# Performance work log

Measured on AMD Instinct MI355X. Metric: run time of the kernel, lower is better.

The kernel has to match this reference:

```python
import jax, jax.numpy as jnp
import numpy as np
from jax import lax

WS = 8        # window size
NH = 4        # num heads
HD = 32       # head dim
DIM = NH * HD # 128
SCALE = HD ** -0.5


def _rel_index(ws):
    coords = np.stack(np.meshgrid(np.arange(ws), np.arange(ws), indexing='ij'))  # (2,ws,ws)
    cf = coords.reshape(2, -1)                      # (2, N)
    rel = cf[:, :, None] - cf[:, None, :]           # (2, N, N)
    rel = rel.transpose(1, 2, 0).astype(np.int64)   # (N, N, 2)
    rel[..., 0] += ws - 1
    rel[..., 1] += ws - 1
    rel[..., 0] *= 2 * ws - 1
    return jnp.asarray(rel.sum(-1))                 # (N, N)


def setup_inputs() -> dict:
    key = jax.random.key(0)
    ks = jax.random.split(key, 8)
    B, H, W = 8, 128, 128
    return {
        'x': jax.random.normal(ks[0], (B, DIM, H, W), jnp.float32),
        'qkv_w': jax.random.normal(ks[1], (DIM, 3 * DIM), jnp.float32) * 0.02,
        'qkv_b': jnp.zeros((3 * DIM,), jnp.float32),
        'proj_w': jax.random.normal(ks[2], (DIM, DIM), jnp.float32) * 0.02,
        'proj_b': jnp.zeros((DIM,), jnp.float32),
        'rpb_table': jax.random.normal(ks[3], ((2 * WS - 1) * (2 * WS - 1), NH), jnp.float32) * 0.02,
        'fc_w': jax.random.normal(ks[4], (9, 3 * NH), jnp.float32) * 0.1,   # 1x1 conv: (out=9, in=3*NH)
        'fc_b': jnp.zeros((9,), jnp.float32),
        'dep_w': jax.random.normal(ks[5], (DIM, 9, 3, 3), jnp.float32) * 0.1,  # grouped conv OIHW, groups=HD
        'dep_b': jnp.zeros((DIM,), jnp.float32),
        'rate1': jnp.array(0.5, jnp.float32),
        'rate2': jnp.array(0.5, jnp.float32),
    }


def reference(x, qkv_w, qkv_b, proj_w, proj_b, rpb_table, fc_w, fc_b, dep_w, dep_b, rate1, rate2):
    B, C, H, W = x.shape
    N = WS * WS
    xh = jnp.transpose(x, (0, 2, 3, 1))                 # (B,H,W,C)
    qkv = xh @ qkv_w + qkv_b                            # (B,H,W,3C)

    # ----- conv branch -----
    f_all = qkv.reshape(B, H * W, 3 * NH, HD).transpose(0, 2, 1, 3)       # (B,3NH,HW,HD)
    f_c = jnp.einsum('oc,bcnd->bond', fc_w, f_all) + fc_b[None, :, None, None]  # (B,9,HW,HD)
    f_conv = jnp.transpose(f_c, (0, 3, 1, 2)).reshape(B, HD * 9, H, W)    # (B,9*HD,H,W)
    out_conv = lax.conv_general_dilated(
        f_conv, dep_w, window_strides=(1, 1), padding=((1, 1), (1, 1)),
        dimension_numbers=('NCHW', 'OIHW', 'NCHW'), feature_group_count=HD)
    out_conv = jnp.transpose(out_conv + dep_b[None, :, None, None], (0, 2, 3, 1))  # (B,H,W,C)

    # ----- windowed attention branch -----
    nWh, nWw = H // WS, W // WS
    w = qkv.reshape(B, nWh, WS, nWw, WS, 3 * C).transpose(0, 1, 3, 2, 4, 5)
    w = w.reshape(B * nWh * nWw, N, 3, NH, HD).transpose(2, 0, 3, 1, 4)   # (3,Bw,NH,N,HD)
    q, k, v = w[0] * SCALE, w[1], w[2]
    attn = jnp.einsum('bhnd,bhmd->bhnm', q, k)                            # (Bw,NH,N,N)
    bias = rpb_table[_rel_index(WS)]                                      # (N,N,NH)
    attn = attn + jnp.transpose(bias, (2, 0, 1))[None]
    attn = jax.nn.softmax(attn, axis=-1)
    xa = jnp.einsum('bhnm,bhmd->bnhd', attn, v).reshape(-1, N, C)         # (Bw,N,C)
    xa = xa @ proj_w + proj_b
    xa = xa.reshape(B, nWh, nWw, WS, WS, C).transpose(0, 1, 3, 2, 4, 5).reshape(B, H, W, C)

    out = rate1 * xa + rate2 * out_conv
    return jnp.transpose(out, (0, 3, 1, 2))
```

## Files before the change

kernel.cpp:

```cpp
#include <hip/hip_runtime.h>

typedef unsigned short ushort_t;
typedef unsigned int uint_t;
typedef __attribute__((ext_vector_type(8))) short short8;
typedef __attribute__((ext_vector_type(4))) float f32x4;

#define SCALE 0.17677669529663687f

__device__ __forceinline__ float blo(uint_t u) { return __uint_as_float(u << 16); }
__device__ __forceinline__ float bhi(uint_t u) { return __uint_as_float(u & 0xffff0000u); }
__device__ __forceinline__ float u2f(ushort_t u) { return __uint_as_float(((uint_t)u) << 16); }
__device__ __forceinline__ ushort_t f2u(float f) {
    const uint_t x = __float_as_uint(f);
    return (ushort_t)((x + 0x7fffu + ((x >> 16) & 1u)) >> 16);
}
__device__ __forceinline__ uint_t pack2(float a, float b) {
    return (uint_t)f2u(a) | ((uint_t)f2u(b) << 16);
}

__device__ __forceinline__ float dot8(const float* qa, uint4 u) {
    return qa[0] * blo(u.x) + qa[1] * bhi(u.x) + qa[2] * blo(u.y) + qa[3] * bhi(u.y)
         + qa[4] * blo(u.z) + qa[5] * bhi(u.z) + qa[6] * blo(u.w) + qa[7] * bhi(u.w);
}
__device__ __forceinline__ void pv8(float* a, float e, uint4 u) {
    a[0] += e * blo(u.x); a[1] += e * bhi(u.x); a[2] += e * blo(u.y); a[3] += e * bhi(u.y);
    a[4] += e * blo(u.z); a[5] += e * bhi(u.z); a[6] += e * blo(u.w); a[7] += e * bhi(u.w);
}


__global__ __launch_bounds__(256) void k_qqkv(
    const float* __restrict__ x, const float* __restrict__ w,
    const float* __restrict__ wb, ushort_t* __restrict__ qkv)
{
    __shared__ ushort_t XT[128 * 128];
    __shared__ ushort_t WT[128 * 128];
    const int t = threadIdx.x;
    const int p0 = blockIdx.x * 128;
    const int b = p0 >> 14;
    const int rem = p0 & 16383;
    const float* xb = x + ((size_t)b << 21) + rem;

#pragma unroll
    for (int it = 0; it < 8; ++it) {
        const int slot = it * 256 + t;
        const int p = slot & 127, cb = slot >> 7;
        uint4 u;
        {
            const float a0 = xb[(size_t)(cb * 8 + 0) * 16384 + p];
            const float a1 = xb[(size_t)(cb * 8 + 1) * 16384 + p];
            const float a2 = xb[(size_t)(cb * 8 + 2) * 16384 + p];
            const float a3 = xb[(size_t)(cb * 8 + 3) * 16384 + p];
            const float a4 = xb[(size_t)(cb * 8 + 4) * 16384 + p];
            const float a5 = xb[(size_t)(cb * 8 + 5) * 16384 + p];
            const float a6 = xb[(size_t)(cb * 8 + 6) * 16384 + p];
            const float a7 = xb[(size_t)(cb * 8 + 7) * 16384 + p];
            u.x = pack2(a0, a1); u.y = pack2(a2, a3);
            u.z = pack2(a4, a5); u.w = pack2(a6, a7);
        }
        *(uint4*)&XT[p * 128 + ((cb ^ (p & 7)) << 3)] = u;
    }

    const int l = t & 63, wv = t >> 6;
    const int wj = (wv >> 1) * 64, wp = (wv & 1) * 64;
    const int lr = l & 15, lg = l >> 4;

    for (int jt = 0; jt < 3; ++jt) {
        const int j0 = jt * 128;
        __syncthreads();

#pragma unroll
        for (int it = 0; it < 8; ++it) {
            const int slot = it * 256 + t;
            const int j = slot & 127, cb = slot >> 7;
            uint4 u;
            {
                const float a0 = w[(size_t)(cb * 8 + 0) * 384 + j0 + j];
                const float a1 = w[(size_t)(cb * 8 + 1) * 384 + j0 + j];
                const float a2 = w[(size_t)(cb * 8 + 2) * 384 + j0 + j];
                const float a3 = w[(size_t)(cb * 8 + 3) * 384 + j0 + j];
                const float a4 = w[(size_t)(cb * 8 + 4) * 384 + j0 + j];
                const float a5 = w[(size_t)(cb * 8 + 5) * 384 + j0 + j];
                const float a6 = w[(size_t)(cb * 8 + 6) * 384 + j0 + j];
                const float a7 = w[(size_t)(cb * 8 + 7) * 384 + j0 + j];
                u.x = pack2(a0, a1); u.y = pack2(a2, a3);
                u.z = pack2(a4, a5); u.w = pack2(a6, a7);
            }
            *(uint4*)&WT[j * 128 + ((cb ^ (j & 7)) << 3)] = u;
        }
        __syncthreads();

        f32x4 acc[4][4];
#pragma unroll
        for (int i = 0; i < 4; ++i)
#pragma unroll
            for (int j = 0; j < 4; ++j) acc[i][j] = (f32x4){0.f, 0.f, 0.f, 0.f};

#pragma unroll
        for (int ks = 0; ks < 4; ++ks) {
            const int kb = ks * 4 + lg;
            short8 af[4], bf[4];
#pragma unroll
            for (int i = 0; i < 4; ++i) {
                const int jr = wj + i * 16 + lr;
                af[i] = *(const short8*)&WT[jr * 128 + ((kb ^ (jr & 7)) << 3)];
                const int pr = wp + i * 16 + lr;
                bf[i] = *(const short8*)&XT[pr * 128 + ((kb ^ (pr & 7)) << 3)];
            }
#pragma unroll
            for (int ji = 0; ji < 4; ++ji)
#pragma unroll
                for (int pi = 0; pi < 4; ++pi)
                    acc[ji][pi] = __builtin_amdgcn_mfma_f32_16x16x32_bf16(
                        af[ji], bf[pi], acc[ji][pi], 0, 0, 0);
        }
        __syncthreads();

#pragma unroll
        for (int ji = 0; ji < 4; ++ji) {
            const int jq = wj + ji * 16 + 4 * lg;
            const float4 bias = *(const float4*)&wb[j0 + jq];
#pragma unroll
            for (int pi = 0; pi < 4; ++pi) {
                const int p = wp + pi * 16 + lr;
                uint2 o;
                o.x = pack2(acc[ji][pi][0] + bias.x, acc[ji][pi][1] + bias.y);
                o.y = pack2(acc[ji][pi][2] + bias.z, acc[ji][pi][3] + bias.w);
                *(uint2*)&WT[p * 128 + (((jq >> 3) ^ (p & 7)) << 3) + (jq & 7)] = o;
            }
        }
        __syncthreads();

#pragma unroll
        for (int it = 0; it < 8; ++it) {
            const int slot = it * 256 + t;
            const int seg = slot & 15, p = slot >> 4;
            const uint4 v = *(const uint4*)&WT[p * 128 + ((seg ^ (p & 7)) << 3)];
            *(uint4*)&qkv[(size_t)(p0 + p) * 384 + j0 + seg * 8] = v;
        }
    }
}

__global__ __launch_bounds__(256, 4) void k_attn3(
    const ushort_t* __restrict__ qkv, const float* __restrict__ rpb,
    float* __restrict__ out)
{
    __shared__ float arena[9604];
    uint_t* kv32 = (uint_t*)arena;
    float* rpbl = arena + 8704;
    const int t = threadIdx.x;
    const int b = blockIdx.x >> 8, wy = (blockIdx.x >> 4) & 15, wx = blockIdx.x & 15;
    const int prow0 = (b << 14) + (wy * 8) * 128 + wx * 8;
    const uint_t* qkvu = (const uint_t*)qkv;

    for (int i = t; i < 4096; i += 256) {
        const int m = i >> 6, u = i & 63;
        const size_t pr = (size_t)(prow0 + (m >> 3) * 128 + (m & 7)) * 192;
        kv32[m * 68 + u]        = qkvu[pr + 64 + u];
        kv32[4352 + m * 68 + u] = qkvu[pr + 128 + u];
    }
    for (int i = t; i < 900; i += 256) rpbl[i] = rpb[i];

    const int h = t >> 6, n = t & 63;
    const size_t pq = (size_t)(prow0 + (n >> 3) * 128 + (n & 7)) * 192;
    float qa[32];
    const uint_t* qrow = qkvu + pq + h * 16;
#pragma unroll
    for (int j = 0; j < 16; ++j) {
        const uint_t u = qrow[j];
        qa[2 * j]     = blo(u) * SCALE;
        qa[2 * j + 1] = bhi(u) * SCALE;
    }
    __syncthreads();

    const int ry = n >> 3, rx = n & 7;
    const float* rpbl_t = rpbl + h;
    const int rbase = (ry + 7) * 15 + (rx + 7);

    const uint_t* kbase = kv32 + h * 16;
    const uint_t* vbase = kv32 + 4352 + h * 16;

    float mx = -1e30f, l = 0.f;
    float acc[32];
#pragma unroll
    for (int cc = 0; cc < 32; ++cc) acc[cc] = 0.f;

#pragma unroll 4
    for (int m = 0; m < 64; ++m) {
        const uint4* kr = (const uint4*)(kbase + m * 68);
        const uint4 k0 = kr[0], k1 = kr[1], k2 = kr[2], k3 = kr[3];
        float s = (dot8(qa, k0) + dot8(qa + 8, k1))
                + (dot8(qa + 16, k2) + dot8(qa + 24, k3));
        s += rpbl_t[4 * (rbase - (m >> 3) * 15 - (m & 7))];
        if (s > mx) {
            const float sc = __expf(mx - s);
            mx = s;
            l *= sc;
#pragma unroll
            for (int cc = 0; cc < 32; ++cc) acc[cc] *= sc;
        }
        const float e = __expf(s - mx);
        l += e;
        const uint4* vr = (const uint4*)(vbase + m * 68);
        const uint4 v0 = vr[0], v1 = vr[1], v2 = vr[2], v3 = vr[3];
        pv8(acc, e, v0); pv8(acc + 8, e, v1);
        pv8(acc + 16, e, v2); pv8(acc + 24, e, v3);
    }
    const float inv = 1.f / l;

    const int oy = wy * 8 + ry, ox = wx * 8 + rx;
    float* ob = out + ((size_t)b << 21) + (size_t)(oy * 128 + ox);
#pragma unroll
    for (int cc = 0; cc < 32; ++cc)
        ob[(size_t)(h * 32 + cc) << 14] = acc[cc] * inv;
}

__global__ __launch_bounds__(256) void k_proj(
    const float* __restrict__ pw, const float* __restrict__ pb,
    const float* __restrict__ r1, float* __restrict__ out)
{
    __shared__ ushort_t XT[128 * 128];
    __shared__ ushort_t WT[128 * 128];
    const int t = threadIdx.x;
    const int p0 = blockIdx.x * 128;
    const int b = p0 >> 14;
    const int rem = p0 & 16383;
    const float* xb = out + ((size_t)b << 21) + rem;

#pragma unroll
    for (int it = 0; it < 8; ++it) {
        const int slot = it * 256 + t;
        const int p = slot & 127, cb = slot >> 7;
        uint4 u;
        {
            const float a0 = xb[(size_t)(cb * 8 + 0) * 16384 + p];
            const float a1 = xb[(size_t)(cb * 8 + 1) * 16384 + p];
            const float a2 = xb[(size_t)(cb * 8 + 2) * 16384 + p];
            const float a3 = xb[(size_t)(cb * 8 + 3) * 16384 + p];
            const float a4 = xb[(size_t)(cb * 8 + 4) * 16384 + p];
            const float a5 = xb[(size_t)(cb * 8 + 5) * 16384 + p];
            const float a6 = xb[(size_t)(cb * 8 + 6) * 16384 + p];
            const float a7 = xb[(size_t)(cb * 8 + 7) * 16384 + p];
            u.x = pack2(a0, a1); u.y = pack2(a2, a3);
            u.z = pack2(a4, a5); u.w = pack2(a6, a7);
        }
        *(uint4*)&XT[p * 128 + ((cb ^ (p & 7)) << 3)] = u;
    }
#pragma unroll
    for (int it = 0; it < 8; ++it) {
        const int slot = it * 256 + t;
        const int j = slot & 127, cb = slot >> 7;
        uint4 u;
        {
            const float a0 = pw[(size_t)(cb * 8 + 0) * 128 + j];
            const float a1 = pw[(size_t)(cb * 8 + 1) * 128 + j];
            const float a2 = pw[(size_t)(cb * 8 + 2) * 128 + j];
            const float a3 = pw[(size_t)(cb * 8 + 3) * 128 + j];
            const float a4 = pw[(size_t)(cb * 8 + 4) * 128 + j];
            const float a5 = pw[(size_t)(cb * 8 + 5) * 128 + j];
            const float a6 = pw[(size_t)(cb * 8 + 6) * 128 + j];
            const float a7 = pw[(size_t)(cb * 8 + 7) * 128 + j];
            u.x = pack2(a0, a1); u.y = pack2(a2, a3);
            u.z = pack2(a4, a5); u.w = pack2(a6, a7);
        }
        *(uint4*)&WT[j * 128 + ((cb ^ (j & 7)) << 3)] = u;
    }
    __syncthreads();

    const int l = t & 63, wv = t >> 6;
    const int wj = (wv >> 1) * 64, wp = (wv & 1) * 64;
    const int lr = l & 15, lg = l >> 4;

    f32x4 acc[4][4];
#pragma unroll
    for (int i = 0; i < 4; ++i)
#pragma unroll
        for (int j = 0; j < 4; ++j) acc[i][j] = (f32x4){0.f, 0.f, 0.f, 0.f};

#pragma unroll
    for (int ks = 0; ks < 4; ++ks) {
        const int kb = ks * 4 + lg;
        short8 af[4], bf[4];
#pragma unroll
        for (int i = 0; i < 4; ++i) {
            const int jr = wj + i * 16 + lr;
            af[i] = *(const short8*)&WT[jr * 128 + ((kb ^ (jr & 7)) << 3)];
            const int pr = wp + i * 16 + lr;
            bf[i] = *(const short8*)&XT[pr * 128 + ((kb ^ (pr & 7)) << 3)];
        }
#pragma unroll
        for (int ji = 0; ji < 4; ++ji)
#pragma unroll
            for (int pi = 0; pi < 4; ++pi)
                acc[ji][pi] = __builtin_amdgcn_mfma_f32_16x16x32_bf16(
                    af[ji], bf[pi], acc[ji][pi], 0, 0, 0);
    }

    const float rate1 = r1[0];
    float* obase = out + ((size_t)b << 21) + rem;
#pragma unroll
    for (int ji = 0; ji < 4; ++ji) {
        const int jq = wj + ji * 16 + 4 * lg;
        const float4 bias = *(const float4*)&pb[jq];
#pragma unroll
        for (int pi = 0; pi < 4; ++pi) {
            const int p = wp + pi * 16 + lr;
            float* op = obase + (size_t)jq * 16384 + p;
            op[0]     = rate1 * (acc[ji][pi][0] + bias.x);
            op[16384] = rate1 * (acc[ji][pi][1] + bias.y);
            op[32768] = rate1 * (acc[ji][pi][2] + bias.z);
            op[49152] = rate1 * (acc[ji][pi][3] + bias.w);
        }
    }
}

__global__ __launch_bounds__(256) void k_conv2(
    const ushort_t* __restrict__ qkv, const float* __restrict__ fcw,
    const float* __restrict__ fcb, const float* __restrict__ depw,
    const float* __restrict__ depb, const float* __restrict__ r2,
    float* __restrict__ out)
{
    __shared__ float fcl[11664];
    __shared__ __align__(16) float dwl[1296];
    __shared__ float fcwl[108];
    __shared__ float fcbl[9];

    const int t = threadIdx.x;
    const int b = blockIdx.x >> 6, tile = blockIdx.x & 63;
    const int ty0 = (tile >> 3) << 4, tx0 = (tile & 7) << 4;
    if (t < 108) fcwl[t] = fcw[t];
    if (t < 9)   fcbl[t] = fcb[t];
    const float rate2 = r2[0];
    const int py = t >> 4, px = t & 15;
    float* ob = out + ((size_t)b << 21) + (size_t)((ty0 + py) * 128 + (tx0 + px));

    const int row0 = t / 18, col0 = t - row0 * 18;
    const int hy0 = ty0 + row0 - 1, hx0 = tx0 + col0 - 1;
    const int g0 = ((unsigned)hy0 < 128u && (unsigned)hx0 < 128u)
                       ? ((b << 14) + hy0 * 128 + hx0) : -1;
    const int t1 = t + 256, row1 = t1 / 18, col1 = t1 - row1 * 18;
    const int hy1 = ty0 + row1 - 1, hx1 = tx0 + col1 - 1;
    const int g1 = (t < 68 && (unsigned)hy1 < 128u && (unsigned)hx1 < 128u)
                       ? ((b << 14) + hy1 * 128 + hx1) : -1;

    for (int chunk = 0; chunk < 8; ++chunk) {
        __syncthreads();
        for (int i = t; i < 1296; i += 256)
            dwl[i] = depw[(chunk * 16 + (i & 15)) * 81 + (i >> 4)];

#pragma unroll
        for (int half = 0; half < 2; ++half) {
            const int g = half ? g1 : g0;
            const int pix = half ? (256 + t) : t;
            if (half && t >= 68) break;
            float fo[9][4];
#pragma unroll
            for (int ii = 0; ii < 9; ++ii) {
                const float bv = (g >= 0) ? fcbl[ii] : 0.f;
                fo[ii][0] = bv; fo[ii][1] = bv; fo[ii][2] = bv; fo[ii][3] = bv;
            }
            if (g >= 0) {
                const uint2* qp = (const uint2*)(qkv + (size_t)g * 384 + chunk * 4);
#pragma unroll
                for (int e = 0; e < 12; ++e) {
                    const uint2 q = qp[e * 8];
                    const float f0 = blo(q.x), f1 = bhi(q.x);
                    const float f2 = blo(q.y), f3 = bhi(q.y);
#pragma unroll
                    for (int ii = 0; ii < 9; ++ii) {
                        const float wv = fcwl[ii * 12 + e];
                        fo[ii][0] += wv * f0; fo[ii][1] += wv * f1;
                        fo[ii][2] += wv * f2; fo[ii][3] += wv * f3;
                    }
                }
            }
#pragma unroll
            for (int ii = 0; ii < 9; ++ii)
#pragma unroll
                for (int dd = 0; dd < 4; ++dd)
                    fcl[(ii * 4 + dd) * 324 + pix] = fo[ii][dd];
        }
        __syncthreads();

        float4 accv[4];
#pragma unroll
        for (int dd = 0; dd < 4; ++dd) accv[dd] = make_float4(0.f, 0.f, 0.f, 0.f);
#pragma unroll
        for (int ii = 0; ii < 9; ++ii) {
#pragma unroll
            for (int kk = 0; kk < 9; ++kk) {
                const int ky = kk / 3, kx = kk - (kk / 3) * 3;
                const int hpix = (py + ky) * 18 + px + kx;
                const float4* dwp = (const float4*)&dwl[(ii * 9 + kk) * 16];
#pragma unroll
                for (int dd = 0; dd < 4; ++dd) {
                    const float f = fcl[(ii * 4 + dd) * 324 + hpix];
                    const float4 d4 = dwp[dd];
                    accv[dd].x += f * d4.x; accv[dd].y += f * d4.y;
                    accv[dd].z += f * d4.z; accv[dd].w += f * d4.w;
                }
            }
        }
#pragma unroll
        for (int dd = 0; dd < 4; ++dd) {
            const float av[4] = {accv[dd].x, accv[dd].y, accv[dd].z, accv[dd].w};
#pragma unroll
            for (int j = 0; j < 4; ++j) {
                const int oc = chunk * 16 + dd * 4 + j;
                ob[(size_t)oc << 14] += rate2 * (av[j] + depb[oc]);
            }
        }
    }
}

#define WS_W2  0
#define WS_B2  36864
#define WS_TOT 37152

__global__ __launch_bounds__(256) void k_prep_f(
    const float* __restrict__ qkv_w, const float* __restrict__ qkv_b,
    const float* __restrict__ fcw, const float* __restrict__ fcb,
    float* __restrict__ ws)
{
    const int idx = blockIdx.x * 256 + threadIdx.x;
    if (idx < WS_B2) {
        const int c = idx / 288, r = idx - c * 288, i = r >> 5, d = r & 31;
        float s = 0.f;
#pragma unroll
        for (int e = 0; e < 12; ++e)
            s += fcw[i * 12 + e] * qkv_w[c * 384 + e * 32 + d];
        ws[idx] = s;
    } else if (idx < WS_TOT) {
        const int r = idx - WS_B2, i = r >> 5, d = r & 31;
        float s = fcb[i];
#pragma unroll
        for (int e = 0; e < 12; ++e)
            s += fcw[i * 12 + e] * qkv_b[e * 32 + d];
        ws[idx] = s;
    }
}

__global__ __launch_bounds__(256) void k_attn_f(
    const float* __restrict__ x, const float* __restrict__ qw,
    const float* __restrict__ qb, const float* __restrict__ pw,
    const float* __restrict__ pb, const float* __restrict__ rpb,
    const float* __restrict__ r1, float* __restrict__ out)
{
    __shared__ ushort_t xw[8192];
    __shared__ float arena[8450];
    ushort_t* kvb = (ushort_t*)arena;
    const int t = threadIdx.x;
    const int b = blockIdx.x >> 8, wy = (blockIdx.x >> 4) & 15, wx = blockIdx.x & 15;
    const size_t xbase = ((size_t)b << 21) + (size_t)((wy * 8) * 128 + wx * 8);
    for (int i = t; i < 8192; i += 256) {
        const int c = i >> 6, p = i & 63;
        xw[i] = f2u(x[xbase + (size_t)c * 16384 + (p >> 3) * 128 + (p & 7)]);
    }
    __syncthreads();
    const int h = t >> 6, n = t & 63;
    float qa[32], ka[32], va[32];
#pragma unroll
    for (int cc = 0; cc < 32; ++cc) {
        qa[cc] = qb[h * 32 + cc];
        ka[cc] = qb[128 + h * 32 + cc];
        va[cc] = qb[256 + h * 32 + cc];
    }
    const float* wbase = qw + h * 32;
    for (int c = 0; c < 128; ++c) {
        const float xv = u2f(xw[c * 64 + n]);
        const float* wr = wbase + c * 384;
#pragma unroll
        for (int j = 0; j < 8; ++j) {
            const float4 aq = ((const float4*)wr)[j];
            const float4 ak = ((const float4*)(wr + 128))[j];
            const float4 av = ((const float4*)(wr + 256))[j];
            qa[4 * j + 0] += xv * aq.x; qa[4 * j + 1] += xv * aq.y;
            qa[4 * j + 2] += xv * aq.z; qa[4 * j + 3] += xv * aq.w;
            ka[4 * j + 0] += xv * ak.x; ka[4 * j + 1] += xv * ak.y;
            ka[4 * j + 2] += xv * ak.z; ka[4 * j + 3] += xv * ak.w;
            va[4 * j + 0] += xv * av.x; va[4 * j + 1] += xv * av.y;
            va[4 * j + 2] += xv * av.z; va[4 * j + 3] += xv * av.w;
        }
    }
#pragma unroll
    for (int cc = 0; cc < 32; ++cc) qa[cc] *= SCALE;
    uint_t* kv32 = (uint_t*)kvb;
#pragma unroll
    for (int j = 0; j < 16; ++j) {
        kv32[n * 66 + h * 16 + j] = pack2(ka[2 * j], ka[2 * j + 1]);
        kv32[4224 + n * 66 + h * 16 + j] = pack2(va[2 * j], va[2 * j + 1]);
    }
    __syncthreads();
    const int ry = n >> 3, rx = n & 7;
    float sar[64];
    float mx = -1e30f;
#pragma unroll
    for (int m = 0; m < 64; ++m) {
        const uint2* kr = (const uint2*)(kvb + m * 132 + h * 32);
        float s = 0.f;
#pragma unroll
        for (int j = 0; j < 8; ++j) {
            const uint2 u = kr[j];
            s += qa[4 * j + 0] * blo(u.x) + qa[4 * j + 1] * bhi(u.x)
               + qa[4 * j + 2] * blo(u.y) + qa[4 * j + 3] * bhi(u.y);
        }
        s += rpb[((ry - (m >> 3) + 7) * 15 + (rx - (m & 7) + 7)) * 4 + h];
        sar[m] = s;
        mx = fmaxf(mx, s);
    }
    float l = 0.f;
#pragma unroll
    for (int m = 0; m < 64; ++m) { const float e = __expf(sar[m] - mx); sar[m] = e; l += e; }
    const float inv = 1.f / l;
    float acc[32];
#pragma unroll
    for (int cc = 0; cc < 32; ++cc) acc[cc] = 0.f;
#pragma unroll
    for (int m = 0; m < 64; ++m) {
        const float pm = sar[m];
        const uint2* vr = (const uint2*)(kvb + 8448 + m * 132 + h * 32);
#pragma unroll
        for (int j = 0; j < 8; ++j) {
            const uint2 u = vr[j];
            acc[4 * j + 0] += pm * blo(u.x); acc[4 * j + 1] += pm * bhi(u.x);
            acc[4 * j + 2] += pm * blo(u.y); acc[4 * j + 3] += pm * bhi(u.y);
        }
    }
    __syncthreads();
#pragma unroll
    for (int cc = 0; cc < 32; ++cc) arena[n * 130 + h * 32 + cc] = acc[cc] * inv;
    __syncthreads();
    const int p = t & 63, jb = t >> 6;
    float aj[32];
#pragma unroll
    for (int jj = 0; jj < 32; ++jj) aj[jj] = pb[jb * 32 + jj];
    const float* xr = arena + p * 130;
    const float* pwb = pw + jb * 32;
    for (int c = 0; c < 128; ++c) {
        const float xv = xr[c];
        const float4* pr = (const float4*)(pwb + c * 128);
#pragma unroll
        for (int j = 0; j < 8; ++j) {
            const float4 w4 = pr[j];
            aj[4 * j + 0] += xv * w4.x; aj[4 * j + 1] += xv * w4.y;
            aj[4 * j + 2] += xv * w4.z; aj[4 * j + 3] += xv * w4.w;
        }
    }
    const float rate1 = r1[0];
    const int oy = wy * 8 + (p >> 3), ox = wx * 8 + (p & 7);
    float* ob = out + ((size_t)b << 21) + (size_t)(oy * 128 + ox);
#pragma unroll
    for (int jj = 0; jj < 32; ++jj)
        ob[(size_t)(jb * 32 + jj) << 14] = rate1 * aj[jj];
}

__global__ __launch_bounds__(256) void k_conv_f(
    const float* __restrict__ x, const float* __restrict__ ws,
    const float* __restrict__ depw, const float* __restrict__ depb,
    const float* __restrict__ r2, float* __restrict__ out)
{
    __shared__ float arena[12960];
    __shared__ float b2s[36];
    float* w2l = arena;
    ushort_t* xl = (ushort_t*)(arena + 4608);
    float* fcl = arena;
    float* dwl = arena + 11664;
    const int t = threadIdx.x;
    const int b = blockIdx.x >> 6, tile = blockIdx.x & 63;
    const int ty0 = (tile >> 3) << 4, tx0 = (tile & 7) << 4;
    const size_t xbase = ((size_t)b << 21);
    const float rate2 = r2[0];
    const int py = t >> 4, px = t & 15;
    float* ob = out + ((size_t)b << 21) + (size_t)((ty0 + py) * 128 + (tx0 + px));
    const int r0 = t / 18, c0 = t - r0 * 18;
    const bool ok0 = ((unsigned)(ty0 + r0 - 1) < 128u) && ((unsigned)(tx0 + c0 - 1) < 128u);
    const int t1 = 256 + t, r1i = t1 / 18, c1 = t1 - r1i * 18;
    const bool ok1 = (t < 68) && ((unsigned)(ty0 + r1i - 1) < 128u) && ((unsigned)(tx0 + c1 - 1) < 128u);
    for (int chunk = 0; chunk < 8; ++chunk) {
        __syncthreads();
        for (int i = t; i < 4608; i += 256) {
            const int c = i / 36, r = i - c * 36;
            w2l[i] = ws[WS_W2 + c * 288 + (r >> 2) * 32 + chunk * 4 + (r & 3)];
        }
        if (t < 36) b2s[t] = ws[WS_B2 + (t >> 2) * 32 + chunk * 4 + (t & 3)];
        __syncthreads();
        float fca[2][36];
#pragma unroll
        for (int r = 0; r < 36; ++r) { fca[0][r] = b2s[r]; fca[1][r] = b2s[r]; }
        for (int cs = 0; cs < 8; ++cs) {
            if (cs) __syncthreads();
            for (int i = t; i < 5184; i += 256) {
                const int cc = i / 324, pp = i - cc * 324;
                const int row = pp / 18, col = pp - row * 18;
                const int hy = ty0 + row - 1, hx = tx0 + col - 1;
                ushort_t v = 0;
                if ((unsigned)hy < 128u && (unsigned)hx < 128u)
                    v = f2u(x[xbase + (size_t)(cs * 16 + cc) * 16384 + hy * 128 + hx]);
                xl[i] = v;
            }
            __syncthreads();
#pragma unroll 4
            for (int cc = 0; cc < 16; ++cc) {
                const float xv0 = u2f(xl[cc * 324 + t]);
                const float xv1 = (t < 68) ? u2f(xl[cc * 324 + 256 + t]) : 0.f;
                const float* wr = w2l + (cs * 16 + cc) * 36;
#pragma unroll
                for (int r = 0; r < 36; r += 4) {
                    const float4 w4 = *(const float4*)(wr + r);
                    fca[0][r + 0] += xv0 * w4.x; fca[0][r + 1] += xv0 * w4.y;
                    fca[0][r + 2] += xv0 * w4.z; fca[0][r + 3] += xv0 * w4.w;
                    fca[1][r + 0] += xv1 * w4.x; fca[1][r + 1] += xv1 * w4.y;
                    fca[1][r + 2] += xv1 * w4.z; fca[1][r + 3] += xv1 * w4.w;
                }
            }
        }
        __syncthreads();
#pragma unroll
        for (int r = 0; r < 36; ++r) {
            fcl[r * 324 + t] = ok0 ? fca[0][r] : 0.f;
            if (t < 68) fcl[r * 324 + 256 + t] = ok1 ? fca[1][r] : 0.f;
        }
        for (int i = t; i < 1296; i += 256) {
            const int kk = i >> 4, ocl = i & 15;
            dwl[i] = depw[(chunk * 16 + ocl) * 81 + kk];
        }
        __syncthreads();
        float4 accv[4];
#pragma unroll
        for (int dd = 0; dd < 4; ++dd) accv[dd] = make_float4(0.f, 0.f, 0.f, 0.f);
#pragma unroll
        for (int ii = 0; ii < 9; ++ii) {
#pragma unroll
            for (int kk = 0; kk < 9; ++kk) {
                const int ky = kk / 3, kx = kk - (kk / 3) * 3;
                const int hpix = (py + ky) * 18 + px + kx;
                const float4* dwp = (const float4*)&dwl[(ii * 9 + kk) * 16];
#pragma unroll
                for (int dd = 0; dd < 4; ++dd) {
                    const float f = fcl[(ii * 4 + dd) * 324 + hpix];
                    const float4 d4 = dwp[dd];
                    accv[dd].x += f * d4.x; accv[dd].y += f * d4.y;
                    accv[dd].z += f * d4.z; accv[dd].w += f * d4.w;
                }
            }
        }
#pragma unroll
        for (int dd = 0; dd < 4; ++dd) {
            const float av[4] = {accv[dd].x, accv[dd].y, accv[dd].z, accv[dd].w};
#pragma unroll
            for (int j = 0; j < 4; ++j) {
                const int oc = chunk * 16 + dd * 4 + j;
                ob[(size_t)oc << 14] += rate2 * (av[j] + depb[oc]);
            }
        }
    }
}

extern "C" void kernel_launch(void* const* d_in, const int* in_sizes, int n_in,
                              void* d_out, int out_size, void* d_ws, size_t ws_size,
                              hipStream_t stream) {
    (void)in_sizes; (void)n_in; (void)out_size;
    const float* x      = (const float*)d_in[0];
    const float* qkv_w  = (const float*)d_in[1];
    const float* qkv_b  = (const float*)d_in[2];
    const float* proj_w = (const float*)d_in[3];
    const float* proj_b = (const float*)d_in[4];
    const float* rpb    = (const float*)d_in[5];
    const float* fc_w   = (const float*)d_in[6];
    const float* fc_b   = (const float*)d_in[7];
    const float* dep_w  = (const float*)d_in[8];
    const float* dep_b  = (const float*)d_in[9];
    const float* rate1  = (const float*)d_in[10];
    const float* rate2  = (const float*)d_in[11];
    float* out = (float*)d_out;

    if (ws_size >= (size_t)131072 * 384 * 2) {
        ushort_t* qkv = (ushort_t*)d_ws;
        k_qqkv<<<dim3(1024), dim3(256), 0, stream>>>(x, qkv_w, qkv_b, qkv);
        k_attn3<<<dim3(2048), dim3(256), 0, stream>>>(qkv, rpb, out);
        k_proj<<<dim3(1024), dim3(256), 0, stream>>>(proj_w, proj_b, rate1, out);
        k_conv2<<<dim3(512), dim3(256), 0, stream>>>(qkv, fc_w, fc_b, dep_w,
                                                     dep_b, rate2, out);
    } else {
        float* wsf = (float*)d_ws;
        k_prep_f<<<dim3(146), dim3(256), 0, stream>>>(qkv_w, qkv_b, fc_w, fc_b, wsf);
        k_attn_f<<<dim3(2048), dim3(256), 0, stream>>>(x, qkv_w, qkv_b, proj_w,
                                                       proj_b, rpb, rate1, out);
        k_conv_f<<<dim3(512), dim3(256), 0, stream>>>(x, wsf, dep_w, dep_b,
                                                      rate2, out);
    }
}
```

Measured before the change: 496.2 us.

## Restructure conv kernel with smaller tiles, LDS-staged qkv halo, and more blocks

The depthwise-conv kernel now uses 4x16 pixel tiles with 512 threads and 2048 blocks, up from 16x16 tiles with 256 threads and 512 blocks. Each block loads its whole qkv halo (72 pixels x 384 bf16) into shared memory once with coalesced 16-byte loads, instead of reading scattered 8-byte global loads in every channel chunk. The fc mixing and the conv accumulation are spread over more threads, with two output channels per thread. In exchange, halo overhead per tile is larger (18x6 halo for 64 outputs versus 18x18 for 256) and the kernel needs about 100KB of LDS per block, which limits occupancy.

```diff
diff --git a/kernel.cpp b/kernel.cpp
--- a/kernel.cpp
+++ b/kernel.cpp
@@ -313,102 +313,87 @@
     }
 }
 
-__global__ __launch_bounds__(256) void k_conv2(
+__global__ __launch_bounds__(512) void k_conv3(
     const ushort_t* __restrict__ qkv, const float* __restrict__ fcw,
     const float* __restrict__ fcb, const float* __restrict__ depw,
     const float* __restrict__ depb, const float* __restrict__ r2,
     float* __restrict__ out)
 {
-    __shared__ float fcl[11664];
+    __shared__ ushort_t qbuf[41904];
+    __shared__ float fcl[3888];
     __shared__ __align__(16) float dwl[1296];
     __shared__ float fcwl[108];
     __shared__ float fcbl[9];
 
     const int t = threadIdx.x;
-    const int b = blockIdx.x >> 6, tile = blockIdx.x & 63;
-    const int ty0 = (tile >> 3) << 4, tx0 = (tile & 7) << 4;
+    const int b = blockIdx.x >> 8, tile = blockIdx.x & 255;
+    const int ty0 = (tile >> 3) << 2;
+    const int tx0 = (tile & 7) << 4;
     if (t < 108) fcwl[t] = fcw[t];
-    if (t < 9)   fcbl[t] = fcb[t];
+    else if (t < 117) fcbl[t - 108] = fcb[t - 108];
     const float rate2 = r2[0];
-    const int py = t >> 4, px = t & 15;
-    float* ob = out + ((size_t)b << 21) + (size_t)((ty0 + py) * 128 + (tx0 + px));
-
-    const int row0 = t / 18, col0 = t - row0 * 18;
-    const int hy0 = ty0 + row0 - 1, hx0 = tx0 + col0 - 1;
-    const int g0 = ((unsigned)hy0 < 128u && (unsigned)hx0 < 128u)
-                       ? ((b << 14) + hy0 * 128 + hx0) : -1;
-    const int t1 = t + 256, row1 = t1 / 18, col1 = t1 - row1 * 18;
-    const int hy1 = ty0 + row1 - 1, hx1 = tx0 + col1 - 1;
-    const int g1 = (t < 68 && (unsigned)hy1 < 128u && (unsigned)hx1 < 128u)
-                       ? ((b << 14) + hy1 * 128 + hx1) : -1;
+
+    const uint4* qkv4 = (const uint4*)qkv;
+    for (int i = t; i < 5184; i += 512) {
+        const int row = i / 48, seg = i - row * 48;
+        const int hr = row / 18, hc = row - hr * 18;
+        const int gy = ty0 + hr - 1, gx = tx0 + hc - 1;
+        uint4 v = make_uint4(0u, 0u, 0u, 0u);
+        if ((unsigned)gy < 128u && (unsigned)gx < 128u) {
+            const int g = (b << 14) + gy * 128 + gx;
+            v = qkv4[(size_t)g * 48 + seg];
+        }
+        char* dst = (char*)qbuf + row * 776 + seg * 16;
+        *(uint2*)dst       = make_uint2(v.x, v.y);
+        *(uint2*)(dst + 8) = make_uint2(v.z, v.w);
+    }
+
+    const int op = t & 63, og = t >> 6;
+    const int py = op >> 4, px = op & 15;
+    const int dd_c = og >> 1;
+    const int gy_o = ty0 + py, gx_o = tx0 + px;
+    float* ob = out + ((size_t)b << 21) + (size_t)(gy_o * 128 + gx_o);
 
     for (int chunk = 0; chunk < 8; ++chunk) {
         __syncthreads();
-        for (int i = t; i < 1296; i += 256)
+
+        for (int i = t; i < 1296; i += 512)
             dwl[i] = depw[(chunk * 16 + (i & 15)) * 81 + (i >> 4)];
 
-#pragma unroll
-        for (int half = 0; half < 2; ++half) {
-            const int g = half ? g1 : g0;
-            const int pix = half ? (256 + t) : t;
-            if (half && t >= 68) break;
-            float fo[9][4];
-#pragma unroll
-            for (int ii = 0; ii < 9; ++ii) {
-                const float bv = (g >= 0) ? fcbl[ii] : 0.f;
-                fo[ii][0] = bv; fo[ii][1] = bv; fo[ii][2] = bv; fo[ii][3] = bv;
-            }
-            if (g >= 0) {
-                const uint2* qp = (const uint2*)(qkv + (size_t)g * 384 + chunk * 4);
-#pragma unroll
-                for (int e = 0; e < 12; ++e) {
-                    const uint2 q = qp[e * 8];
-                    const float f0 = blo(q.x), f1 = bhi(q.x);
-                    const float f2 = blo(q.y), f3 = bhi(q.y);
-#pragma unroll
-                    for (int ii = 0; ii < 9; ++ii) {
-                        const float wv = fcwl[ii * 12 + e];
-                        fo[ii][0] += wv * f0; fo[ii][1] += wv * f1;
-                        fo[ii][2] += wv * f2; fo[ii][3] += wv * f3;
-                    }
-                }
-            }
-#pragma unroll
-            for (int ii = 0; ii < 9; ++ii)
-#pragma unroll
-                for (int dd = 0; dd < 4; ++dd)
-                    fcl[(ii * 4 + dd) * 324 + pix] = fo[ii][dd];
-        }
-        __syncthreads();
-
-        float4 accv[4];
-#pragma unroll
-        for (int dd = 0; dd < 4; ++dd) accv[dd] = make_float4(0.f, 0.f, 0.f, 0.f);
+        for (int v = t; v < 972; v += 512) {
+            const int i9 = v / 108, pix = v - i9 * 108;
+            const int hr = pix / 18, hc = pix - hr * 18;
+            const int gy = ty0 + hr - 1, gx = tx0 + hc - 1;
+            const bool inb = ((unsigned)gy < 128u) && ((unsigned)gx < 128u);
+            const float bv = inb ? fcbl[i9] : 0.f;
+            float fo0 = bv, fo1 = bv, fo2 = bv, fo3 = bv;
+            const char* qrow = (const char*)qbuf + pix * 776 + chunk * 8;
+#pragma unroll
+            for (int e = 0; e < 12; ++e) {
+                const uint2 q = *(const uint2*)(qrow + e * 64);
+                const float wv = fcwl[i9 * 12 + e];
+                fo0 += wv * blo(q.x); fo1 += wv * bhi(q.x);
+                fo2 += wv * blo(q.y); fo3 += wv * bhi(q.y);
+            }
+            float* fp = fcl + i9 * 432 + pix;
+            fp[0] = fo0; fp[108] = fo1; fp[216] = fo2; fp[324] = fo3;
+        }
+        __syncthreads();
+
+        float a0 = 0.f, a1 = 0.f;
 #pragma unroll
         for (int ii = 0; ii < 9; ++ii) {
 #pragma unroll
             for (int kk = 0; kk < 9; ++kk) {
                 const int ky = kk / 3, kx = kk - (kk / 3) * 3;
-                const int hpix = (py + ky) * 18 + px + kx;
-                const float4* dwp = (const float4*)&dwl[(ii * 9 + kk) * 16];
-#pragma unroll
-                for (int dd = 0; dd < 4; ++dd) {
-                    const float f = fcl[(ii * 4 + dd) * 324 + hpix];
-                    const float4 d4 = dwp[dd];
-                    accv[dd].x += f * d4.x; accv[dd].y += f * d4.y;
-                    accv[dd].z += f * d4.z; accv[dd].w += f * d4.w;
-                }
-            }
-        }
-#pragma unroll
-        for (int dd = 0; dd < 4; ++dd) {
-            const float av[4] = {accv[dd].x, accv[dd].y, accv[dd].z, accv[dd].w};
-#pragma unroll
-            for (int j = 0; j < 4; ++j) {
-                const int oc = chunk * 16 + dd * 4 + j;
-                ob[(size_t)oc << 14] += rate2 * (av[j] + depb[oc]);
-            }
-        }
+                const float f = fcl[(ii * 4 + dd_c) * 108 + (py + ky) * 18 + px + kx];
+                const float2 w2 = *(const float2*)&dwl[(ii * 9 + kk) * 16 + og * 2];
+                a0 += f * w2.x; a1 += f * w2.y;
+            }
+        }
+        const int oc0 = chunk * 16 + og * 2;
+        ob[(size_t)oc0 << 14]       += rate2 * (a0 + depb[oc0]);
+        ob[(size_t)(oc0 + 1) << 14] += rate2 * (a1 + depb[oc0 + 1]);
     }
 }
 
@@ -678,8 +663,8 @@
         k_qqkv<<<dim3(1024), dim3(256), 0, stream>>>(x, qkv_w, qkv_b, qkv);
         k_attn3<<<dim3(2048), dim3(256), 0, stream>>>(qkv, rpb, out);
         k_proj<<<dim3(1024), dim3(256), 0, stream>>>(proj_w, proj_b, rate1, out);
-        k_conv2<<<dim3(512), dim3(256), 0, stream>>>(qkv, fc_w, fc_b, dep_w,
-                                                     dep_b, rate2, out);
+        k_conv3<<<dim3(2048), dim3(512), 0, stream>>>(qkv, fc_w, fc_b, dep_w,
+                                                      dep_b, rate2, out);
     } else {
         float* wsf = (float*)d_ws;
         k_prep_f<<<dim3(146), dim3(256), 0, stream>>>(qkv_w, qkv_b, fc_w, fc_b, wsf);
```

Result: slower. 602.0 us (+21.3%).

## Retile conv kernel to 8x16 pixel tiles with 32-channel chunks and 16B loads

Applied to the files above, without the earlier changes.

The depthwise-conv branch kernel now processes 8x16 output tiles (1024 blocks instead of 512) and 32 output channels per pass (4 passes instead of 8). Each halo thread loads 16-byte qkv vectors covering 8 head-dim elements, so there are fewer passes over qkv and fewer read-modify-writes of the output. Two thread groups split the 32 channels, each computing 16 outputs per pixel. The cost is a larger halo fraction per tile, only 180 of 256 threads active during the fc stage, and more LDS per block, which may reduce occupancy.

```diff
diff --git a/kernel.cpp b/kernel.cpp
--- a/kernel.cpp
+++ b/kernel.cpp
@@ -313,101 +313,100 @@
     }
 }
 
-__global__ __launch_bounds__(256) void k_conv2(
+__global__ __launch_bounds__(256) void k_conv5(
     const ushort_t* __restrict__ qkv, const float* __restrict__ fcw,
     const float* __restrict__ fcb, const float* __restrict__ depw,
     const float* __restrict__ depb, const float* __restrict__ r2,
     float* __restrict__ out)
 {
-    __shared__ float fcl[11664];
-    __shared__ __align__(16) float dwl[1296];
+    __shared__ float fcl[12960];
+    __shared__ __align__(16) float dwl[2592];
     __shared__ float fcwl[108];
     __shared__ float fcbl[9];
 
     const int t = threadIdx.x;
-    const int b = blockIdx.x >> 6, tile = blockIdx.x & 63;
-    const int ty0 = (tile >> 3) << 4, tx0 = (tile & 7) << 4;
+    const int b = blockIdx.x >> 7, tile = blockIdx.x & 127;
+    const int ty0 = (tile >> 3) << 3;
+    const int tx0 = (tile & 7) << 4;
     if (t < 108) fcwl[t] = fcw[t];
-    if (t < 9)   fcbl[t] = fcb[t];
+    else if (t < 117) fcbl[t - 108] = fcb[t - 108];
     const float rate2 = r2[0];
-    const int py = t >> 4, px = t & 15;
-    float* ob = out + ((size_t)b << 21) + (size_t)((ty0 + py) * 128 + (tx0 + px));
-
-    const int row0 = t / 18, col0 = t - row0 * 18;
-    const int hy0 = ty0 + row0 - 1, hx0 = tx0 + col0 - 1;
-    const int g0 = ((unsigned)hy0 < 128u && (unsigned)hx0 < 128u)
-                       ? ((b << 14) + hy0 * 128 + hx0) : -1;
-    const int t1 = t + 256, row1 = t1 / 18, col1 = t1 - row1 * 18;
-    const int hy1 = ty0 + row1 - 1, hx1 = tx0 + col1 - 1;
-    const int g1 = (t < 68 && (unsigned)hy1 < 128u && (unsigned)hx1 < 128u)
-                       ? ((b << 14) + hy1 * 128 + hx1) : -1;
-
-    for (int chunk = 0; chunk < 8; ++chunk) {
-        __syncthreads();
-        for (int i = t; i < 1296; i += 256)
-            dwl[i] = depw[(chunk * 16 + (i & 15)) * 81 + (i >> 4)];
-
-#pragma unroll
-        for (int half = 0; half < 2; ++half) {
-            const int g = half ? g1 : g0;
-            const int pix = half ? (256 + t) : t;
-            if (half && t >= 68) break;
-            float fo[9][4];
+
+    const int hr = t / 18, hc = t - hr * 18;
+    const int gy = ty0 + hr - 1, gx = tx0 + hc - 1;
+    const bool inb = (t < 180) && ((unsigned)gy < 128u) && ((unsigned)gx < 128u);
+    const int g = inb ? ((b << 14) + gy * 128 + gx) : 0;
+
+    const int op = t & 127, og = t >> 7;
+    const int py = op >> 4, px = op & 15;
+    float* ob = out + ((size_t)b << 21) + (size_t)((ty0 + py) * 128 + tx0 + px);
+
+    const uint4* qkv4 = (const uint4*)qkv;
+
+    for (int cp = 0; cp < 4; ++cp) {
+        __syncthreads();
+
+        for (int i = t; i < 2592; i += 256)
+            dwl[i] = depw[(cp * 32 + (i & 31)) * 81 + (i >> 5)];
+
+        if (t < 180) {
+            float fo[9][8];
 #pragma unroll
             for (int ii = 0; ii < 9; ++ii) {
-                const float bv = (g >= 0) ? fcbl[ii] : 0.f;
-                fo[ii][0] = bv; fo[ii][1] = bv; fo[ii][2] = bv; fo[ii][3] = bv;
-            }
-            if (g >= 0) {
-                const uint2* qp = (const uint2*)(qkv + (size_t)g * 384 + chunk * 4);
+                const float bv = inb ? fcbl[ii] : 0.f;
+#pragma unroll
+                for (int dd = 0; dd < 8; ++dd) fo[ii][dd] = bv;
+            }
+            if (inb) {
+                const uint4* qp = qkv4 + (size_t)g * 48 + cp;
 #pragma unroll
                 for (int e = 0; e < 12; ++e) {
-                    const uint2 q = qp[e * 8];
+                    const uint4 q = qp[e * 4];
                     const float f0 = blo(q.x), f1 = bhi(q.x);
                     const float f2 = blo(q.y), f3 = bhi(q.y);
+                    const float f4 = blo(q.z), f5 = bhi(q.z);
+                    const float f6 = blo(q.w), f7 = bhi(q.w);
 #pragma unroll
                     for (int ii = 0; ii < 9; ++ii) {
                         const float wv = fcwl[ii * 12 + e];
                         fo[ii][0] += wv * f0; fo[ii][1] += wv * f1;
                         fo[ii][2] += wv * f2; fo[ii][3] += wv * f3;
+                        fo[ii][4] += wv * f4; fo[ii][5] += wv * f5;
+                        fo[ii][6] += wv * f6; fo[ii][7] += wv * f7;
                     }
                 }
             }
 #pragma unroll
             for (int ii = 0; ii < 9; ++ii)
 #pragma unroll
-                for (int dd = 0; dd < 4; ++dd)
-                    fcl[(ii * 4 + dd) * 324 + pix] = fo[ii][dd];
-        }
-        __syncthreads();
-
-        float4 accv[4];
-#pragma unroll
-        for (int dd = 0; dd < 4; ++dd) accv[dd] = make_float4(0.f, 0.f, 0.f, 0.f);
+                for (int dd = 0; dd < 8; ++dd)
+                    fcl[(ii * 8 + dd) * 180 + t] = fo[ii][dd];
+        }
+        __syncthreads();
+
+        float a[16];
+#pragma unroll
+        for (int j = 0; j < 16; ++j) a[j] = 0.f;
 #pragma unroll
         for (int ii = 0; ii < 9; ++ii) {
 #pragma unroll
             for (int kk = 0; kk < 9; ++kk) {
                 const int ky = kk / 3, kx = kk - (kk / 3) * 3;
-                const int hpix = (py + ky) * 18 + px + kx;
-                const float4* dwp = (const float4*)&dwl[(ii * 9 + kk) * 16];
-#pragma unroll
-                for (int dd = 0; dd < 4; ++dd) {
-                    const float f = fcl[(ii * 4 + dd) * 324 + hpix];
-                    const float4 d4 = dwp[dd];
-                    accv[dd].x += f * d4.x; accv[dd].y += f * d4.y;
-                    accv[dd].z += f * d4.z; accv[dd].w += f * d4.w;
-                }
-            }
-        }
-#pragma unroll
-        for (int dd = 0; dd < 4; ++dd) {
-            const float av[4] = {accv[dd].x, accv[dd].y, accv[dd].z, accv[dd].w};
-#pragma unroll
-            for (int j = 0; j < 4; ++j) {
-                const int oc = chunk * 16 + dd * 4 + j;
-                ob[(size_t)oc << 14] += rate2 * (av[j] + depb[oc]);
-            }
+                const int hp = (py + ky) * 18 + px + kx;
+                const float* fp = &fcl[(ii * 8 + og * 4) * 180 + hp];
+                const float f0 = fp[0], f1 = fp[180], f2 = fp[360], f3 = fp[540];
+                const float4* dw = (const float4*)&dwl[(ii * 9 + kk) * 32 + og * 16];
+                const float4 w0 = dw[0], w1 = dw[1], w2 = dw[2], w3 = dw[3];
+                a[0]  += f0 * w0.x; a[1]  += f0 * w0.y; a[2]  += f0 * w0.z; a[3]  += f0 * w0.w;
+                a[4]  += f1 * w1.x; a[5]  += f1 * w1.y; a[6]  += f1 * w1.z; a[7]  += f1 * w1.w;
+                a[8]  += f2 * w2.x; a[9]  += f2 * w2.y; a[10] += f2 * w2.z; a[11] += f2 * w2.w;
+                a[12] += f3 * w3.x; a[13] += f3 * w3.y; a[14] += f3 * w3.z; a[15] += f3 * w3.w;
+            }
+        }
+#pragma unroll
+        for (int j = 0; j < 16; ++j) {
+            const int oc = cp * 32 + og * 16 + j;
+            ob[(size_t)oc << 14] += rate2 * (a[j] + depb[oc]);
         }
     }
 }
@@ -678,8 +677,8 @@
         k_qqkv<<<dim3(1024), dim3(256), 0, stream>>>(x, qkv_w, qkv_b, qkv);
         k_attn3<<<dim3(2048), dim3(256), 0, stream>>>(qkv, rpb, out);
         k_proj<<<dim3(1024), dim3(256), 0, stream>>>(proj_w, proj_b, rate1, out);
-        k_conv2<<<dim3(512), dim3(256), 0, stream>>>(qkv, fc_w, fc_b, dep_w,
-                                                     dep_b, rate2, out);
+        k_conv5<<<dim3(1024), dim3(256), 0, stream>>>(qkv, fc_w, fc_b, dep_w,
+                                                      dep_b, rate2, out);
     } else {
         float* wsf = (float*)d_ws;
         k_prep_f<<<dim3(146), dim3(256), 0, stream>>>(qkv_w, qkv_b, fc_w, fc_b, wsf);
```

After: 535.7 us. 8.0% more time.

## Rewrite window attention with bf16 MFMA for QK^T and PV

Applied to the files above, without the earlier changes.

Replaces the scalar per-thread online-softmax attention loop with matrix-core MFMA 16x16x32 bf16 instructions for both the score and the value products. Q and K are staged in LDS, V is stored transposed, and scores are kept in registers for a two-pass softmax with cross-lane shuffles. The probabilities are then written back to LDS as bf16 for the PV MFMA. This is meant to remove the heavy scalar FMA cost of the attention kernel. In exchange it uses more LDS, drops the occupancy hint, and rounds the probabilities to bf16.

```diff
diff --git a/kernel.cpp b/kernel.cpp
--- a/kernel.cpp
+++ b/kernel.cpp
@@ -140,13 +140,13 @@
     }
 }
 
-__global__ __launch_bounds__(256, 4) void k_attn3(
+__global__ __launch_bounds__(256) void k_attn4(
     const ushort_t* __restrict__ qkv, const float* __restrict__ rpb,
     float* __restrict__ out)
 {
-    __shared__ float arena[9604];
-    uint_t* kv32 = (uint_t*)arena;
-    float* rpbl = arena + 8704;
+    __shared__ uint_t lds[13956];
+    ushort_t* lds_sh = (ushort_t*)lds;
+    float* rpbl = (float*)(lds + 13056);
     const int t = threadIdx.x;
     const int b = blockIdx.x >> 8, wy = (blockIdx.x >> 4) & 15, wx = blockIdx.x & 15;
     const int prow0 = (b << 14) + (wy * 8) * 128 + wx * 8;
@@ -155,63 +155,130 @@
     for (int i = t; i < 4096; i += 256) {
         const int m = i >> 6, u = i & 63;
         const size_t pr = (size_t)(prow0 + (m >> 3) * 128 + (m & 7)) * 192;
-        kv32[m * 68 + u]        = qkvu[pr + 64 + u];
-        kv32[4352 + m * 68 + u] = qkvu[pr + 128 + u];
+        lds[m * 68 + u]        = qkvu[pr + u];
+        lds[4352 + m * 68 + u] = qkvu[pr + 64 + u];
+        const uint_t v = qkvu[pr + 128 + u];
+        lds_sh[17408 + (2 * u) * 68 + m]     = (ushort_t)(v & 0xffffu);
+        lds_sh[17408 + (2 * u + 1) * 68 + m] = (ushort_t)(v >> 16);
     }
     for (int i = t; i < 900; i += 256) rpbl[i] = rpb[i];
-
-    const int h = t >> 6, n = t & 63;
-    const size_t pq = (size_t)(prow0 + (n >> 3) * 128 + (n & 7)) * 192;
-    float qa[32];
-    const uint_t* qrow = qkvu + pq + h * 16;
-#pragma unroll
-    for (int j = 0; j < 16; ++j) {
-        const uint_t u = qrow[j];
-        qa[2 * j]     = blo(u) * SCALE;
-        qa[2 * j + 1] = bhi(u) * SCALE;
-    }
     __syncthreads();
 
-    const int ry = n >> 3, rx = n & 7;
-    const float* rpbl_t = rpbl + h;
-    const int rbase = (ry + 7) * 15 + (rx + 7);
-
-    const uint_t* kbase = kv32 + h * 16;
-    const uint_t* vbase = kv32 + 4352 + h * 16;
-
-    float mx = -1e30f, l = 0.f;
-    float acc[32];
-#pragma unroll
-    for (int cc = 0; cc < 32; ++cc) acc[cc] = 0.f;
-
-#pragma unroll 4
-    for (int m = 0; m < 64; ++m) {
-        const uint4* kr = (const uint4*)(kbase + m * 68);
-        const uint4 k0 = kr[0], k1 = kr[1], k2 = kr[2], k3 = kr[3];
-        float s = (dot8(qa, k0) + dot8(qa + 8, k1))
-                + (dot8(qa + 16, k2) + dot8(qa + 24, k3));
-        s += rpbl_t[4 * (rbase - (m >> 3) * 15 - (m & 7))];
-        if (s > mx) {
-            const float sc = __expf(mx - s);
-            mx = s;
-            l *= sc;
-#pragma unroll
-            for (int cc = 0; cc < 32; ++cc) acc[cc] *= sc;
-        }
-        const float e = __expf(s - mx);
-        l += e;
-        const uint4* vr = (const uint4*)(vbase + m * 68);
-        const uint4 v0 = vr[0], v1 = vr[1], v2 = vr[2], v3 = vr[3];
-        pv8(acc, e, v0); pv8(acc + 8, e, v1);
-        pv8(acc + 16, e, v2); pv8(acc + 24, e, v3);
-    }
-    const float inv = 1.f / l;
-
-    const int oy = wy * 8 + ry, ox = wx * 8 + rx;
-    float* ob = out + ((size_t)b << 21) + (size_t)(oy * 128 + ox);
-#pragma unroll
-    for (int cc = 0; cc < 32; ++cc)
-        ob[(size_t)(h * 32 + cc) << 14] = acc[cc] * inv;
+    const int h = t >> 6, l = t & 63;
+    const int lr = l & 15, lg = l >> 4;
+
+    short8 af_k[4], bf_q[4];
+#pragma unroll
+    for (int i = 0; i < 4; ++i) {
+        af_k[i] = *(const short8*)&lds_sh[8704 + (i * 16 + lr) * 136 + h * 32 + lg * 8];
+        bf_q[i] = *(const short8*)&lds_sh[(i * 16 + lr) * 136 + h * 32 + lg * 8];
+    }
+    f32x4 sA[4][4];
+#pragma unroll
+    for (int nt = 0; nt < 4; ++nt)
+#pragma unroll
+        for (int mt = 0; mt < 4; ++mt)
+            sA[nt][mt] = __builtin_amdgcn_mfma_f32_16x16x32_bf16(
+                af_k[mt], bf_q[nt], (f32x4){0.f, 0.f, 0.f, 0.f}, 0, 0, 0);
+
+    float inv[4];
+#pragma unroll
+    for (int nt = 0; nt < 4; ++nt) {
+        const int n = nt * 16 + lr;
+        const int ry = n >> 3, rx = n & 7;
+        float mxv = -1e30f;
+#pragma unroll
+        for (int mt = 0; mt < 4; ++mt)
+#pragma unroll
+            for (int r = 0; r < 4; ++r) {
+                const int m = mt * 16 + lg * 4 + r;
+                const float bias =
+                    rpbl[((ry - (m >> 3) + 7) * 15 + (rx - (m & 7) + 7)) * 4 + h];
+                const float s = sA[nt][mt][r] * SCALE + bias;
+                sA[nt][mt][r] = s;
+                mxv = fmaxf(mxv, s);
+            }
+        mxv = fmaxf(mxv, __shfl_xor(mxv, 16));
+        mxv = fmaxf(mxv, __shfl_xor(mxv, 32));
+        float ls = 0.f;
+#pragma unroll
+        for (int mt = 0; mt < 4; ++mt)
+#pragma unroll
+            for (int r = 0; r < 4; ++r) {
+                const float e = __expf(sA[nt][mt][r] - mxv);
+                sA[nt][mt][r] = e;
+                ls += e;
+            }
+        ls += __shfl_xor(ls, 16);
+        ls += __shfl_xor(ls, 32);
+        inv[nt] = 1.f / ls;
+    }
+
+    __syncthreads();
+
+    uint_t* Pb = lds + h * 2176;
+#pragma unroll
+    for (int nt = 0; nt < 4; ++nt) {
+        const int n = nt * 16 + lr;
+#pragma unroll
+        for (int mt = 0; mt < 4; ++mt) {
+            uint2 o;
+            o.x = pack2(sA[nt][mt][0], sA[nt][mt][1]);
+            o.y = pack2(sA[nt][mt][2], sA[nt][mt][3]);
+            *(uint2*)&Pb[n * 34 + mt * 8 + lg * 2] = o;
+        }
+    }
+    asm volatile("s_waitcnt lgkmcnt(0)" ::: "memory");
+
+    union U8 { short8 s8; uint2 u2[2]; };
+    f32x4 oA[2][4];
+#pragma unroll
+    for (int dt = 0; dt < 2; ++dt)
+#pragma unroll
+        for (int nt = 0; nt < 4; ++nt) oA[dt][nt] = (f32x4){0.f, 0.f, 0.f, 0.f};
+#pragma unroll
+    for (int ks = 0; ks < 2; ++ks) {
+        const int kb = ks * 4 + lg;
+        short8 av[2], bp[4];
+#pragma unroll
+        for (int dt = 0; dt < 2; ++dt) {
+            U8 u;
+            const int d = h * 32 + dt * 16 + lr;
+            u.u2[0] = *(const uint2*)&lds[8704 + d * 34 + kb * 4];
+            u.u2[1] = *(const uint2*)&lds[8704 + d * 34 + kb * 4 + 2];
+            av[dt] = u.s8;
+        }
+#pragma unroll
+        for (int nt = 0; nt < 4; ++nt) {
+            U8 u;
+            const int n = nt * 16 + lr;
+            u.u2[0] = *(const uint2*)&Pb[n * 34 + kb * 4];
+            u.u2[1] = *(const uint2*)&Pb[n * 34 + kb * 4 + 2];
+            bp[nt] = u.s8;
+        }
+#pragma unroll
+        for (int dt = 0; dt < 2; ++dt)
+#pragma unroll
+            for (int nt = 0; nt < 4; ++nt)
+                oA[dt][nt] = __builtin_amdgcn_mfma_f32_16x16x32_bf16(
+                    av[dt], bp[nt], oA[dt][nt], 0, 0, 0);
+    }
+
+    float* ob = out + ((size_t)b << 21);
+    const int pixbase = (wy * 8) * 128 + wx * 8;
+#pragma unroll
+    for (int dt = 0; dt < 2; ++dt)
+#pragma unroll
+        for (int nt = 0; nt < 4; ++nt) {
+            const int n = nt * 16 + lr;
+            const size_t po = (size_t)(pixbase + (n >> 3) * 128 + (n & 7));
+            const float iv = inv[nt];
+#pragma unroll
+            for (int r = 0; r < 4; ++r) {
+                const int d = h * 32 + dt * 16 + lg * 4 + r;
+                ob[((size_t)d << 14) + po] = oA[dt][nt][r] * iv;
+            }
+        }
 }
 
 __global__ __launch_bounds__(256) void k_proj(
@@ -676,7 +743,7 @@
     if (ws_size >= (size_t)131072 * 384 * 2) {
         ushort_t* qkv = (ushort_t*)d_ws;
         k_qqkv<<<dim3(1024), dim3(256), 0, stream>>>(x, qkv_w, qkv_b, qkv);
-        k_attn3<<<dim3(2048), dim3(256), 0, stream>>>(qkv, rpb, out);
+        k_attn4<<<dim3(2048), dim3(256), 0, stream>>>(qkv, rpb, out);
         k_proj<<<dim3(1024), dim3(256), 0, stream>>>(proj_w, proj_b, rate1, out);
         k_conv2<<<dim3(512), dim3(256), 0, stream>>>(qkv, fc_w, fc_b, dep_w,
                                                      dep_b, rate2, out);
```

Measured after the change: 433.2 us. 1.15x faster.
